# Performance work log

Hardware: AMD Instinct MI355X
Metric: run time of the kernel (lower is better)

## Reference

```python
import jax, jax.numpy as jnp
import numpy as np

N_COARSE = 12500
N_FINE = 50000
MIN_BASIS = 16  # (min(L_in, L_out) + 1) ** 2 with L_in = L_out = 3


def setup_inputs() -> dict:
    key = jax.random.key(0)
    ks = jax.random.split(key, 8)
    return {
        "last_inv": jax.random.normal(ks[0], (N_COARSE, 256), dtype=jnp.float32),
        "cur_inv": jax.random.normal(ks[1], (N_FINE, 256), dtype=jnp.float32),
        "last_equ": jax.random.normal(ks[2], (N_COARSE, 16, 256), dtype=jnp.float32),
        "cur_equ": jax.random.normal(ks[3], (N_FINE, 16, 256), dtype=jnp.float32),
        "upsampling": jax.random.randint(ks[4], (N_FINE,), 0, N_COARSE, dtype=jnp.int32),
        # Linear weights stored as [in, out] (torch weight is [out, in]; x @ W.T == x @ W_in_out)
        "W_last_equ": jax.random.normal(ks[5], (256, 256), dtype=jnp.float32) * 0.02,
        "W_cur_equ": jax.random.normal(ks[6], (256, 256), dtype=jnp.float32) * 0.02,
        "W_mlp": jax.random.normal(ks[7], (768, 512), dtype=jnp.float32) * 0.02,
    }


def reference(last_inv, cur_inv, last_equ, cur_equ, upsampling, W_last_equ, W_cur_equ, W_mlp):
    # nearest_upsample: gather coarse rows up to fine resolution
    li = jnp.take(last_inv, upsampling, axis=0)                 # [N_fine, 256]
    le = jnp.take(last_equ, upsampling, axis=0)[:, :MIN_BASIS]  # [N_fine, 16, 256]
    le = jnp.einsum('nbc,cd->nbd', le, W_last_equ)              # fc_last_equ (no bias)
    ce = jnp.einsum('nbc,cd->nbd', cur_equ[:, :MIN_BASIS], W_cur_equ)  # fc_cur_equ
    equ = (ce * le).mean(axis=1)                                # [N_fine, 256]
    com = jnp.concatenate([li, cur_inv, equ], axis=-1)          # [N_fine, 768]
    return com @ W_mlp                                          # LastUnaryBlock: Linear, no bias
```

## Files before the change

### kernel.cpp

```cpp
#include <hip/hip_runtime.h>
#include <hip/hip_bf16.h>

#define N_COARSE 12500
#define N_FINE   50000

typedef __bf16 bf16x8 __attribute__((ext_vector_type(8)));
typedef __bf16 bf16x4 __attribute__((ext_vector_type(4)));
typedef float  f32x4  __attribute__((ext_vector_type(4)));


__device__ __forceinline__ bf16x8 cvt8(f32x4 x, f32x4 y) {
    bf16x8 r;
    r[0] = (__bf16)x[0]; r[1] = (__bf16)x[1]; r[2] = (__bf16)x[2]; r[3] = (__bf16)x[3];
    r[4] = (__bf16)y[0]; r[5] = (__bf16)y[1]; r[6] = (__bf16)y[2]; r[7] = (__bf16)y[3];
    return r;
}

__device__ __forceinline__ void lds_barrier() {
    asm volatile("s_waitcnt lgkmcnt(0)" ::: "memory");
    __builtin_amdgcn_s_barrier();
}

__device__ __forceinline__ int swz(int row, int byte) { return byte ^ ((row & 7) << 4); }

__device__ __forceinline__ void st_a(__bf16* lds, int row, int cs, bf16x8 v) {
    *(bf16x8*)((char*)lds + swz(row, row * 512 + cs * 16)) = v;
}
__device__ __forceinline__ bf16x8 ld_a(const __bf16* lds, int row, int ka) {
    return *(const bf16x8*)((const char*)lds + swz(row, row * 512 + ka * 2));
}

template<int NT>
__device__ __forceinline__ void stage_f32(const float* __restrict__ A, long row0,
                                          __bf16* lds, int tid, long maxrow) {
    const int r0 = tid >> 5, cs = tid & 31;
    constexpr int RPI = NT / 32;
    #pragma unroll
    for (int i = 0; i < 64 / RPI; ++i) {
        int row = r0 + i * RPI;
        long gr = row0 + row; if (gr > maxrow) gr = maxrow;
        const float* p = A + gr * 256 + cs * 8;
        f32x4 x = *(const f32x4*)p, y = *(const f32x4*)(p + 4);
        st_a(lds, row, cs, cvt8(x, y));
    }
}

__device__ __forceinline__ void mfma_tile(const __bf16* lds, const bf16x8* __restrict__ packB,
                                          int N, int c0, int ksb,
                                          f32x4 (&acc)[4][4], int lane) {
    const int g = lane >> 4, r15 = lane & 15;
    #pragma unroll
    for (int ks = 0; ks < 8; ++ks) {
        bf16x8 a[4];
        #pragma unroll
        for (int rt = 0; rt < 4; ++rt)
            a[rt] = ld_a(lds, rt * 16 + r15, ks * 32 + g * 8);
        const size_t kb = (size_t)((ksb + ks) * 4 + g) * N;
        #pragma unroll
        for (int ct = 0; ct < 4; ++ct) {
            bf16x8 b = packB[kb + c0 + ct * 16 + r15];
            #pragma unroll
            for (int rt = 0; rt < 4; ++rt)
                acc[rt][ct] = __builtin_amdgcn_mfma_f32_16x16x32_bf16(a[rt], b, acc[rt][ct], 0, 0, 0);
        }
    }
}

__global__ __launch_bounds__(256) void k_pack(const float* __restrict__ W,
                                              __bf16* __restrict__ dst, int K, int N) {
    int idx = blockIdx.x * 256 + threadIdx.x;
    if (idx >= K * N) return;
    int k = idx / N, n = idx % N;
    dst[((size_t)(k >> 3) * N + n) * 8 + (k & 7)] = (__bf16)W[(size_t)k * N + n];
}

__global__ __launch_bounds__(256) void k_cvt(const float* __restrict__ src,
                                             __bf16* __restrict__ dst, int n4) {
    int i = blockIdx.x * 256 + threadIdx.x;
    if (i >= n4) return;
    f32x4 v = ((const f32x4*)src)[i];
    bf16x4 o;
    o[0] = (__bf16)v[0]; o[1] = (__bf16)v[1]; o[2] = (__bf16)v[2]; o[3] = (__bf16)v[3];
    ((bf16x4*)dst)[i] = o;
}

__global__ __launch_bounds__(256) void k_coarse_equ(
    const float* __restrict__ last_equ, const bf16x8* __restrict__ packW,
    __bf16* __restrict__ LEp)
{
    __shared__ __attribute__((aligned(16))) __bf16 As[64 * 256];
    const int tid = threadIdx.x, lane = tid & 63, wid = tid >> 6;
    const long row0 = (long)blockIdx.x * 64;
    stage_f32<256>(last_equ, row0, As, tid, (long)N_COARSE * 16 - 1);
    lds_barrier();
    f32x4 acc[4][4] = {};
    mfma_tile(As, packW, 256, wid * 64, 0, acc, lane);
    #pragma unroll
    for (int rt = 0; rt < 4; ++rt) {
        int coarse = (int)(row0 >> 4) + rt;
        #pragma unroll
        for (int ct = 0; ct < 4; ++ct) {
            int cg = wid * 4 + ct;
            bf16x4 v;
            v[0] = (__bf16)acc[rt][ct][0]; v[1] = (__bf16)acc[rt][ct][1];
            v[2] = (__bf16)acc[rt][ct][2]; v[3] = (__bf16)acc[rt][ct][3];
            *(bf16x4*)(LEp + ((size_t)(coarse * 16 + cg) * 64 + lane) * 4) = v;
        }
    }
}

__global__ __launch_bounds__(256) void k_fine_equ(
    const float* __restrict__ cur_equ, const bf16x8* __restrict__ packW,
    const __bf16* __restrict__ LEp, const int* __restrict__ up,
    __bf16* __restrict__ equ)
{
    __shared__ __attribute__((aligned(16))) __bf16 As[64 * 256];
    const int tid = threadIdx.x, lane = tid & 63, wid = tid >> 6;
    const int n0 = blockIdx.x * 4;
    const long row0 = (long)blockIdx.x * 64;

    int cu[4];
    #pragma unroll
    for (int rt = 0; rt < 4; ++rt) cu[rt] = up[n0 + rt];

    stage_f32<256>(cur_equ, row0, As, tid, (long)N_FINE * 16 - 1);

    __builtin_amdgcn_sched_barrier(0);

    bf16x4 le[4][4];
    #pragma unroll
    for (int rt = 0; rt < 4; ++rt)
        #pragma unroll
        for (int ct = 0; ct < 4; ++ct)
            le[rt][ct] = *(const bf16x4*)(LEp +
                ((size_t)(cu[rt] * 16 + wid * 4 + ct) * 64 + lane) * 4);

    lds_barrier();
    f32x4 acc[4][4] = {};
    mfma_tile(As, packW, 256, wid * 64, 0, acc, lane);

    #pragma unroll
    for (int rt = 0; rt < 4; ++rt) {
        int n = n0 + rt;
        #pragma unroll
        for (int ct = 0; ct < 4; ++ct) {
            float s = acc[rt][ct][0] * (float)le[rt][ct][0]
                    + acc[rt][ct][1] * (float)le[rt][ct][1]
                    + acc[rt][ct][2] * (float)le[rt][ct][2]
                    + acc[rt][ct][3] * (float)le[rt][ct][3];
            s += __shfl_xor(s, 16, 64);
            s += __shfl_xor(s, 32, 64);
            if (lane < 16)
                equ[(size_t)n * 256 + wid * 64 + ct * 16 + lane] = (__bf16)(s * 0.0625f);
        }
    }
}

__global__ __launch_bounds__(512) void k_out(
    const __bf16* __restrict__ li_bf, const float* __restrict__ cur_inv,
    const __bf16* __restrict__ equ, const bf16x8* __restrict__ packW,
    const int* __restrict__ up, float* __restrict__ out)
{
    __shared__ __attribute__((aligned(16))) __bf16 As[64 * 256];
    const int tid = threadIdx.x, lane = tid & 63, wid = tid >> 6;
    const int row0 = blockIdx.x * 64;
    const int c0 = wid * 64;
    const int r0 = tid >> 5, cs = tid & 31;
    f32x4 acc[4][4] = {};

    #pragma unroll
    for (int i = 0; i < 4; ++i) {
        int row = r0 + i * 16;
        int gr = row0 + row; if (gr > N_FINE - 1) gr = N_FINE - 1;
        st_a(As, row, cs, *(const bf16x8*)(li_bf + (size_t)up[gr] * 256 + cs * 8));
    }
    lds_barrier();
    mfma_tile(As, packW, 512, c0, 0, acc, lane);
    lds_barrier();

    stage_f32<512>(cur_inv, row0, As, tid, N_FINE - 1);
    lds_barrier();
    mfma_tile(As, packW, 512, c0, 8, acc, lane);
    lds_barrier();

    #pragma unroll
    for (int i = 0; i < 4; ++i) {
        int row = r0 + i * 16;
        int gr = row0 + row; if (gr > N_FINE - 1) gr = N_FINE - 1;
        st_a(As, row, cs, *(const bf16x8*)(equ + (size_t)gr * 256 + cs * 8));
    }
    lds_barrier();
    mfma_tile(As, packW, 512, c0, 16, acc, lane);

    const int g = lane >> 4, r15 = lane & 15;
    #pragma unroll
    for (int rt = 0; rt < 4; ++rt)
        #pragma unroll
        for (int j = 0; j < 4; ++j) {
            int r = row0 + rt * 16 + g * 4 + j;
            if (r < N_FINE)
                #pragma unroll
                for (int ct = 0; ct < 4; ++ct)
                    out[(size_t)r * 512 + c0 + ct * 16 + r15] = acc[rt][ct][j];
        }
}

extern "C" void kernel_launch(void* const* d_in, const int* in_sizes, int n_in,
                              void* d_out, int out_size, void* d_ws, size_t ws_size,
                              hipStream_t stream) {
    const float* last_inv = (const float*)d_in[0];
    const float* cur_inv  = (const float*)d_in[1];
    const float* last_equ = (const float*)d_in[2];
    const float* cur_equ  = (const float*)d_in[3];
    const int*   up       = (const int*)d_in[4];
    const float* W_le     = (const float*)d_in[5];
    const float* W_ce     = (const float*)d_in[6];
    const float* W_mlp    = (const float*)d_in[7];
    float* out = (float*)d_out;

    char* w = (char*)d_ws;
    __bf16* LEp    = (__bf16*)w;  w += (size_t)N_COARSE * 16 * 256 * 2;
    __bf16* equ    = (__bf16*)w;  w += (size_t)N_FINE * 256 * 2;
    __bf16* li_bf  = (__bf16*)w;  w += (size_t)N_COARSE * 256 * 2;
    __bf16* packLE = (__bf16*)w;  w += (size_t)256 * 256 * 2;
    __bf16* packCE = (__bf16*)w;  w += (size_t)256 * 256 * 2;
    __bf16* packM  = (__bf16*)w;  w += (size_t)768 * 512 * 2;

    k_pack<<<256, 256, 0, stream>>>(W_le, packLE, 256, 256);
    k_pack<<<256, 256, 0, stream>>>(W_ce, packCE, 256, 256);
    k_pack<<<1536, 256, 0, stream>>>(W_mlp, packM, 768, 512);
    k_cvt<<<3125, 256, 0, stream>>>(last_inv, li_bf, N_COARSE * 256 / 4);

    k_coarse_equ<<<N_COARSE * 16 / 64, 256, 0, stream>>>(
        last_equ, (const bf16x8*)packLE, LEp);

    k_fine_equ<<<N_FINE / 4, 256, 0, stream>>>(
        cur_equ, (const bf16x8*)packCE, LEp, up, equ);

    k_out<<<(N_FINE + 63) / 64, 512, 0, stream>>>(
        li_bf, cur_inv, equ, (const bf16x8*)packM, up, out);
}
```

Measured before the change: 557.3 us.

## Sort fine points by coarse parent and remap blocks per XCD for LEp locality

Adds a counting sort (zero, histogram, single-block scan, atomic place) that builds a permutation grouping fine points by their coarse parent index. k_fine_equ now processes fine rows in permuted order and maps block IDs so that each XCD gets a contiguous range, which should keep gathered LEp rows in L2 cache. The cost is four extra small kernels, including a serial single-block scan. The cur_equ loads and the equ writes become scattered row gathers rather than contiguous streams.

After: 594.6 us. +6.7%, slower.

```diff
diff --git a/kernel.cpp b/kernel.cpp
--- a/kernel.cpp
+++ b/kernel.cpp
@@ -84,6 +84,49 @@
     ((bf16x4*)dst)[i] = o;
 }
 
+__global__ __launch_bounds__(256) void k_zero(int* __restrict__ cnt, int n) {
+    int i = blockIdx.x * 256 + threadIdx.x;
+    if (i < n) cnt[i] = 0;
+}
+__global__ __launch_bounds__(256) void k_hist(const int* __restrict__ up, int* __restrict__ cnt) {
+    int n = blockIdx.x * 256 + threadIdx.x;
+    if (n < N_FINE) atomicAdd(&cnt[up[n]], 1);
+}
+__global__ __launch_bounds__(1024) void k_scan(const int* __restrict__ cnt,
+                                               int* __restrict__ base) {
+    __shared__ int buf[1024];
+    __shared__ int carry;
+    const int tid = threadIdx.x;
+    if (tid == 0) carry = 0;
+    __syncthreads();
+    for (int c0 = 0; c0 < N_COARSE; c0 += 1024) {
+        int i = c0 + tid;
+        int v = (i < N_COARSE) ? cnt[i] : 0;
+        buf[tid] = v; __syncthreads();
+        #pragma unroll
+        for (int off = 1; off < 1024; off <<= 1) {
+            int t = (tid >= off) ? buf[tid - off] : 0;
+            __syncthreads();
+            buf[tid] += t;
+            __syncthreads();
+        }
+        int total = buf[1023];
+        if (i < N_COARSE) base[i] = carry + buf[tid] - v;
+        __syncthreads();
+        if (tid == 0) carry += total;
+        __syncthreads();
+    }
+}
+__global__ __launch_bounds__(256) void k_place(const int* __restrict__ up,
+                                               int* __restrict__ cursor,
+                                               int* __restrict__ perm) {
+    int n = blockIdx.x * 256 + threadIdx.x;
+    if (n < N_FINE) {
+        int pos = atomicAdd(&cursor[up[n]], 1);
+        perm[pos] = n;
+    }
+}
+
 __global__ __launch_bounds__(256) void k_coarse_equ(
     const float* __restrict__ last_equ, const bf16x8* __restrict__ packW,
     __bf16* __restrict__ LEp)
@@ -112,21 +155,34 @@
 __global__ __launch_bounds__(256) void k_fine_equ(
     const float* __restrict__ cur_equ, const bf16x8* __restrict__ packW,
     const __bf16* __restrict__ LEp, const int* __restrict__ up,
-    __bf16* __restrict__ equ)
+    const int* __restrict__ perm, __bf16* __restrict__ equ)
 {
     __shared__ __attribute__((aligned(16))) __bf16 As[64 * 256];
     const int tid = threadIdx.x, lane = tid & 63, wid = tid >> 6;
-    const int n0 = blockIdx.x * 4;
-    const long row0 = (long)blockIdx.x * 64;
-
-    int cu[4];
-    #pragma unroll
-    for (int rt = 0; rt < 4; ++rt) cu[rt] = up[n0 + rt];
-
-    stage_f32<256>(cur_equ, row0, As, tid, (long)N_FINE * 16 - 1);
+
+    const int q = N_FINE / 4 / 8, r = N_FINE / 4 % 8;
+    int xcd = blockIdx.x & 7, idx = blockIdx.x >> 3;
+    int wg = (xcd < r ? xcd * (q + 1) : r * (q + 1) + (xcd - r) * q) + idx;
+
+    const int n0 = wg * 4;
+    int pn[4], cu[4];
+    #pragma unroll
+    for (int rt = 0; rt < 4; ++rt) pn[rt] = perm[n0 + rt];
+    #pragma unroll
+    for (int rt = 0; rt < 4; ++rt) cu[rt] = up[pn[rt]];
+
+    const int r0 = tid >> 5, cs = tid & 31;
+    #pragma unroll
+    for (int rt = 0; rt < 4; ++rt)
+        #pragma unroll
+        for (int ii = 0; ii < 2; ++ii) {
+            int row = rt * 16 + ii * 8 + r0;
+            const float* p = cur_equ + ((long)pn[rt] * 16 + ii * 8 + r0) * 256 + cs * 8;
+            f32x4 x = *(const f32x4*)p, y = *(const f32x4*)(p + 4);
+            st_a(As, row, cs, cvt8(x, y));
+        }
 
     __builtin_amdgcn_sched_barrier(0);
-
     bf16x4 le[4][4];
     #pragma unroll
     for (int rt = 0; rt < 4; ++rt)
@@ -141,7 +197,6 @@
 
     #pragma unroll
     for (int rt = 0; rt < 4; ++rt) {
-        int n = n0 + rt;
         #pragma unroll
         for (int ct = 0; ct < 4; ++ct) {
             float s = acc[rt][ct][0] * (float)le[rt][ct][0]
@@ -151,7 +206,8 @@
             s += __shfl_xor(s, 16, 64);
             s += __shfl_xor(s, 32, 64);
             if (lane < 16)
-                equ[(size_t)n * 256 + wid * 64 + ct * 16 + lane] = (__bf16)(s * 0.0625f);
+                equ[(size_t)pn[rt] * 256 + wid * 64 + ct * 16 + lane] =
+                    (__bf16)(s * 0.0625f);
         }
     }
 }
@@ -225,6 +281,14 @@
     __bf16* packLE = (__bf16*)w;  w += (size_t)256 * 256 * 2;
     __bf16* packCE = (__bf16*)w;  w += (size_t)256 * 256 * 2;
     __bf16* packM  = (__bf16*)w;  w += (size_t)768 * 512 * 2;
+    int* cnt    = (int*)w;  w += (size_t)N_COARSE * 4;
+    int* cursor = (int*)w;  w += (size_t)N_COARSE * 4;
+    int* perm   = (int*)w;  w += (size_t)N_FINE * 4;
+
+    k_zero <<<(N_COARSE + 255) / 256, 256, 0, stream>>>(cnt, N_COARSE);
+    k_hist <<<(N_FINE + 255) / 256, 256, 0, stream>>>(up, cnt);
+    k_scan <<<1, 1024, 0, stream>>>(cnt, cursor);
+    k_place<<<(N_FINE + 255) / 256, 256, 0, stream>>>(up, cursor, perm);
 
     k_pack<<<256, 256, 0, stream>>>(W_le, packLE, 256, 256);
     k_pack<<<256, 256, 0, stream>>>(W_ce, packCE, 256, 256);
@@ -235,7 +299,7 @@
         last_equ, (const bf16x8*)packLE, LEp);
 
     k_fine_equ<<<N_FINE / 4, 256, 0, stream>>>(
-        cur_equ, (const bf16x8*)packCE, LEp, up, equ);
+        cur_equ, (const bf16x8*)packCE, LEp, up, perm, equ);
 
     k_out<<<(N_FINE + 63) / 64, 512, 0, stream>>>(
         li_bf, cur_inv, equ, (const bf16x8*)packM, up, out);
```

## Load equ activations directly into MFMA registers, dropping LDS staging

Applied to the files above, without the earlier changes.

The coarse and fine equivariant GEMM kernels no longer stage fp32 activations through LDS with a barrier. Each wave now reads its A fragments straight from global memory, converts them to bf16 in registers, and handles 2 points by 128 output columns, so weight fragments are reused across two points. This removes the LDS round trip and the synchronisation. In exchange, each activation row is read by two waves (one per column half), and the per-lane global loads are less coalesced than the old staged path.

After: 648.3 us (median of 2 runs). +16.3%, slower.

```diff
diff --git a/kernel.cpp b/kernel.cpp
--- a/kernel.cpp
+++ b/kernel.cpp
@@ -22,7 +22,6 @@
 }
 
 __device__ __forceinline__ int swz(int row, int byte) { return byte ^ ((row & 7) << 4); }
-
 __device__ __forceinline__ void st_a(__bf16* lds, int row, int cs, bf16x8 v) {
     *(bf16x8*)((char*)lds + swz(row, row * 512 + cs * 16)) = v;
 }
@@ -88,25 +87,37 @@
     const float* __restrict__ last_equ, const bf16x8* __restrict__ packW,
     __bf16* __restrict__ LEp)
 {
-    __shared__ __attribute__((aligned(16))) __bf16 As[64 * 256];
     const int tid = threadIdx.x, lane = tid & 63, wid = tid >> 6;
-    const long row0 = (long)blockIdx.x * 64;
-    stage_f32<256>(last_equ, row0, As, tid, (long)N_COARSE * 16 - 1);
-    lds_barrier();
-    f32x4 acc[4][4] = {};
-    mfma_tile(As, packW, 256, wid * 64, 0, acc, lane);
-    #pragma unroll
-    for (int rt = 0; rt < 4; ++rt) {
-        int coarse = (int)(row0 >> 4) + rt;
-        #pragma unroll
-        for (int ct = 0; ct < 4; ++ct) {
-            int cg = wid * 4 + ct;
+    const int h = wid & 1, m = wid >> 1;
+    const int c0 = blockIdx.x * 4 + m * 2;
+    const int g = lane >> 4, r15 = lane & 15;
+
+    f32x4 acc[2][8] = {};
+    #pragma unroll
+    for (int ks = 0; ks < 8; ++ks) {
+        bf16x8 b[8];
+        #pragma unroll
+        for (int ct = 0; ct < 8; ++ct)
+            b[ct] = packW[(size_t)(ks * 4 + g) * 256 + h * 128 + ct * 16 + r15];
+        #pragma unroll
+        for (int pt = 0; pt < 2; ++pt) {
+            const float* pa = last_equ +
+                ((size_t)(c0 + pt) * 16 + r15) * 256 + ks * 32 + g * 8;
+            bf16x8 a = cvt8(*(const f32x4*)pa, *(const f32x4*)(pa + 4));
+            #pragma unroll
+            for (int ct = 0; ct < 8; ++ct)
+                acc[pt][ct] = __builtin_amdgcn_mfma_f32_16x16x32_bf16(a, b[ct], acc[pt][ct], 0, 0, 0);
+        }
+    }
+    #pragma unroll
+    for (int pt = 0; pt < 2; ++pt)
+        #pragma unroll
+        for (int ct = 0; ct < 8; ++ct) {
             bf16x4 v;
-            v[0] = (__bf16)acc[rt][ct][0]; v[1] = (__bf16)acc[rt][ct][1];
-            v[2] = (__bf16)acc[rt][ct][2]; v[3] = (__bf16)acc[rt][ct][3];
-            *(bf16x4*)(LEp + ((size_t)(coarse * 16 + cg) * 64 + lane) * 4) = v;
-        }
-    }
+            v[0] = (__bf16)acc[pt][ct][0]; v[1] = (__bf16)acc[pt][ct][1];
+            v[2] = (__bf16)acc[pt][ct][2]; v[3] = (__bf16)acc[pt][ct][3];
+            *(bf16x4*)(LEp + ((size_t)((c0 + pt) * 16 + h * 8 + ct) * 64 + lane) * 4) = v;
+        }
 }
 
 __global__ __launch_bounds__(256) void k_fine_equ(
@@ -114,46 +125,55 @@
     const __bf16* __restrict__ LEp, const int* __restrict__ up,
     __bf16* __restrict__ equ)
 {
-    __shared__ __attribute__((aligned(16))) __bf16 As[64 * 256];
     const int tid = threadIdx.x, lane = tid & 63, wid = tid >> 6;
-    const int n0 = blockIdx.x * 4;
-    const long row0 = (long)blockIdx.x * 64;
-
-    int cu[4];
-    #pragma unroll
-    for (int rt = 0; rt < 4; ++rt) cu[rt] = up[n0 + rt];
-
-    stage_f32<256>(cur_equ, row0, As, tid, (long)N_FINE * 16 - 1);
-
-    __builtin_amdgcn_sched_barrier(0);
-
-    bf16x4 le[4][4];
-    #pragma unroll
-    for (int rt = 0; rt < 4; ++rt)
-        #pragma unroll
-        for (int ct = 0; ct < 4; ++ct)
-            le[rt][ct] = *(const bf16x4*)(LEp +
-                ((size_t)(cu[rt] * 16 + wid * 4 + ct) * 64 + lane) * 4);
-
-    lds_barrier();
-    f32x4 acc[4][4] = {};
-    mfma_tile(As, packW, 256, wid * 64, 0, acc, lane);
-
-    #pragma unroll
-    for (int rt = 0; rt < 4; ++rt) {
-        int n = n0 + rt;
-        #pragma unroll
-        for (int ct = 0; ct < 4; ++ct) {
-            float s = acc[rt][ct][0] * (float)le[rt][ct][0]
-                    + acc[rt][ct][1] * (float)le[rt][ct][1]
-                    + acc[rt][ct][2] * (float)le[rt][ct][2]
-                    + acc[rt][ct][3] * (float)le[rt][ct][3];
+    const int h = wid & 1, m = wid >> 1;
+    const int p0 = blockIdx.x * 4 + m * 2;
+    const int g = lane >> 4, r15 = lane & 15;
+
+    const int cu0 = up[p0], cu1 = up[p0 + 1];
+
+    bf16x4 le[2][8];
+    #pragma unroll
+    for (int ct = 0; ct < 8; ++ct)
+        le[0][ct] = *(const bf16x4*)(LEp +
+            ((size_t)(cu0 * 16 + h * 8 + ct) * 64 + lane) * 4);
+    #pragma unroll
+    for (int ct = 0; ct < 8; ++ct)
+        le[1][ct] = *(const bf16x4*)(LEp +
+            ((size_t)(cu1 * 16 + h * 8 + ct) * 64 + lane) * 4);
+
+    f32x4 acc[2][8] = {};
+    #pragma unroll
+    for (int ks = 0; ks < 8; ++ks) {
+        bf16x8 b[8];
+        #pragma unroll
+        for (int ct = 0; ct < 8; ++ct)
+            b[ct] = packW[(size_t)(ks * 4 + g) * 256 + h * 128 + ct * 16 + r15];
+        #pragma unroll
+        for (int pt = 0; pt < 2; ++pt) {
+            const float* pa = cur_equ +
+                ((size_t)(p0 + pt) * 16 + r15) * 256 + ks * 32 + g * 8;
+            bf16x8 a = cvt8(*(const f32x4*)pa, *(const f32x4*)(pa + 4));
+            #pragma unroll
+            for (int ct = 0; ct < 8; ++ct)
+                acc[pt][ct] = __builtin_amdgcn_mfma_f32_16x16x32_bf16(a, b[ct], acc[pt][ct], 0, 0, 0);
+        }
+    }
+
+    #pragma unroll
+    for (int pt = 0; pt < 2; ++pt)
+        #pragma unroll
+        for (int ct = 0; ct < 8; ++ct) {
+            float s = acc[pt][ct][0] * (float)le[pt][ct][0]
+                    + acc[pt][ct][1] * (float)le[pt][ct][1]
+                    + acc[pt][ct][2] * (float)le[pt][ct][2]
+                    + acc[pt][ct][3] * (float)le[pt][ct][3];
             s += __shfl_xor(s, 16, 64);
             s += __shfl_xor(s, 32, 64);
             if (lane < 16)
-                equ[(size_t)n * 256 + wid * 64 + ct * 16 + lane] = (__bf16)(s * 0.0625f);
-        }
-    }
+                equ[(size_t)(p0 + pt) * 256 + h * 128 + ct * 16 + lane] =
+                    (__bf16)(s * 0.0625f);
+        }
 }
 
 __global__ __launch_bounds__(512) void k_out(
@@ -231,7 +251,7 @@
     k_pack<<<1536, 256, 0, stream>>>(W_mlp, packM, 768, 512);
     k_cvt<<<3125, 256, 0, stream>>>(last_inv, li_bf, N_COARSE * 256 / 4);
 
-    k_coarse_equ<<<N_COARSE * 16 / 64, 256, 0, stream>>>(
+    k_coarse_equ<<<N_COARSE / 4, 256, 0, stream>>>(
         last_equ, (const bf16x8*)packLE, LEp);
 
     k_fine_equ<<<N_FINE / 4, 256, 0, stream>>>(
```

## Double-buffer cur_equ staging in fine equ kernel across multiple sub-tiles

Applied to the files above, without the earlier changes.

The fine equivariant kernel now handles 8 fine points per block in four 32-row sub-tiles. It prefetches the next sub-tile's fp32 rows into registers while running MFMA on the current one, using a ping-pong LDS buffer. Each block pays the weight loads and launch cost over more rows, and LDS use per block is halved, which allows more blocks per CU. The cost is more registers, a barrier per sub-tile, and half as many blocks in the grid.

Result: slower. 630.9 us (+13.2%).

```diff
diff --git a/kernel.cpp b/kernel.cpp
--- a/kernel.cpp
+++ b/kernel.cpp
@@ -22,7 +22,6 @@
 }
 
 __device__ __forceinline__ int swz(int row, int byte) { return byte ^ ((row & 7) << 4); }
-
 __device__ __forceinline__ void st_a(__bf16* lds, int row, int cs, bf16x8 v) {
     *(bf16x8*)((char*)lds + swz(row, row * 512 + cs * 16)) = v;
 }
@@ -109,49 +108,81 @@
     }
 }
 
-__global__ __launch_bounds__(256) void k_fine_equ(
+__global__ __launch_bounds__(256, 4) void k_fine_equ(
     const float* __restrict__ cur_equ, const bf16x8* __restrict__ packW,
     const __bf16* __restrict__ LEp, const int* __restrict__ up,
     __bf16* __restrict__ equ)
 {
-    __shared__ __attribute__((aligned(16))) __bf16 As[64 * 256];
+    __shared__ __attribute__((aligned(16))) __bf16 As[2][32 * 256];
     const int tid = threadIdx.x, lane = tid & 63, wid = tid >> 6;
-    const int n0 = blockIdx.x * 4;
-    const long row0 = (long)blockIdx.x * 64;
-
-    int cu[4];
-    #pragma unroll
-    for (int rt = 0; rt < 4; ++rt) cu[rt] = up[n0 + rt];
-
-    stage_f32<256>(cur_equ, row0, As, tid, (long)N_FINE * 16 - 1);
-
-    __builtin_amdgcn_sched_barrier(0);
-
-    bf16x4 le[4][4];
-    #pragma unroll
-    for (int rt = 0; rt < 4; ++rt)
-        #pragma unroll
-        for (int ct = 0; ct < 4; ++ct)
-            le[rt][ct] = *(const bf16x4*)(LEp +
-                ((size_t)(cu[rt] * 16 + wid * 4 + ct) * 64 + lane) * 4);
-
-    lds_barrier();
-    f32x4 acc[4][4] = {};
-    mfma_tile(As, packW, 256, wid * 64, 0, acc, lane);
-
-    #pragma unroll
-    for (int rt = 0; rt < 4; ++rt) {
-        int n = n0 + rt;
+    const int pbase = blockIdx.x * 8;
+    const int r0 = tid >> 5, cs = tid & 31;
+    const int g = lane >> 4, r15 = lane & 15;
+
+    f32x4 x[4], y[4];
+    #pragma unroll
+    for (int i = 0; i < 4; ++i) {
+        const float* p = cur_equ + ((long)pbase * 16 + i * 8 + r0) * 256 + cs * 8;
+        x[i] = *(const f32x4*)p; y[i] = *(const f32x4*)(p + 4);
+    }
+    #pragma unroll
+    for (int i = 0; i < 4; ++i) st_a(As[0], i * 8 + r0, cs, cvt8(x[i], y[i]));
+
+    #pragma unroll
+    for (int t = 0; t < 4; ++t) {
+        const int cur = t & 1;
+        lds_barrier();
+        if (t < 3) {
+            #pragma unroll
+            for (int i = 0; i < 4; ++i) {
+                const float* p = cur_equ +
+                    ((long)(pbase + (t + 1) * 2) * 16 + i * 8 + r0) * 256 + cs * 8;
+                x[i] = *(const f32x4*)p; y[i] = *(const f32x4*)(p + 4);
+            }
+        }
+        const int p0 = pbase + t * 2;
+        const int cu0 = up[p0], cu1 = up[p0 + 1];
+        bf16x4 le[2][4];
         #pragma unroll
         for (int ct = 0; ct < 4; ++ct) {
-            float s = acc[rt][ct][0] * (float)le[rt][ct][0]
-                    + acc[rt][ct][1] * (float)le[rt][ct][1]
-                    + acc[rt][ct][2] * (float)le[rt][ct][2]
-                    + acc[rt][ct][3] * (float)le[rt][ct][3];
-            s += __shfl_xor(s, 16, 64);
-            s += __shfl_xor(s, 32, 64);
-            if (lane < 16)
-                equ[(size_t)n * 256 + wid * 64 + ct * 16 + lane] = (__bf16)(s * 0.0625f);
+            le[0][ct] = *(const bf16x4*)(LEp +
+                ((size_t)(cu0 * 16 + wid * 4 + ct) * 64 + lane) * 4);
+            le[1][ct] = *(const bf16x4*)(LEp +
+                ((size_t)(cu1 * 16 + wid * 4 + ct) * 64 + lane) * 4);
+        }
+
+        f32x4 acc[2][4] = {};
+        #pragma unroll
+        for (int ks = 0; ks < 8; ++ks) {
+            bf16x8 a0 = ld_a(As[cur], r15,      ks * 32 + g * 8);
+            bf16x8 a1 = ld_a(As[cur], 16 + r15, ks * 32 + g * 8);
+            #pragma unroll
+            for (int ct = 0; ct < 4; ++ct) {
+                bf16x8 b = packW[(size_t)(ks * 4 + g) * 256 + wid * 64 + ct * 16 + r15];
+                acc[0][ct] = __builtin_amdgcn_mfma_f32_16x16x32_bf16(a0, b, acc[0][ct], 0, 0, 0);
+                acc[1][ct] = __builtin_amdgcn_mfma_f32_16x16x32_bf16(a1, b, acc[1][ct], 0, 0, 0);
+            }
+        }
+
+        #pragma unroll
+        for (int pt = 0; pt < 2; ++pt)
+            #pragma unroll
+            for (int ct = 0; ct < 4; ++ct) {
+                float s = acc[pt][ct][0] * (float)le[pt][ct][0]
+                        + acc[pt][ct][1] * (float)le[pt][ct][1]
+                        + acc[pt][ct][2] * (float)le[pt][ct][2]
+                        + acc[pt][ct][3] * (float)le[pt][ct][3];
+                s += __shfl_xor(s, 16, 64);
+                s += __shfl_xor(s, 32, 64);
+                if (lane < 16)
+                    equ[(size_t)(p0 + pt) * 256 + wid * 64 + ct * 16 + lane] =
+                        (__bf16)(s * 0.0625f);
+            }
+
+        if (t < 3) {
+            #pragma unroll
+            for (int i = 0; i < 4; ++i)
+                st_a(As[cur ^ 1], i * 8 + r0, cs, cvt8(x[i], y[i]));
         }
     }
 }
@@ -234,7 +265,7 @@
     k_coarse_equ<<<N_COARSE * 16 / 64, 256, 0, stream>>>(
         last_equ, (const bf16x8*)packLE, LEp);
 
-    k_fine_equ<<<N_FINE / 4, 256, 0, stream>>>(
+    k_fine_equ<<<N_FINE / 8, 256, 0, stream>>>(
         cur_equ, (const bf16x8*)packCE, LEp, up, equ);
 
     k_out<<<(N_FINE + 63) / 64, 512, 0, stream>>>(
```
